# Performance work log

Measured on AMD Instinct MI355X. Metric: run time of the kernel, lower is better.

Reference implementation:

```python
import jax, jax.numpy as jnp
import numpy as np

D_MODEL = 768
D_STATE = 16
K_CONV = 4
BATCH = 2
SEQ = 2048


def setup_inputs() -> dict:
    key = jax.random.key(0)
    ks = jax.random.split(key, 16)
    dm, ds, K = D_MODEL, D_STATE, K_CONV
    s = 0.02
    inp = {
        "x": jax.random.normal(ks[0], (BATCH, SEQ, dm), dtype=jnp.float32),
        # linear weights stored (in, out); y = x @ W + b (equivalent to torch Linear)
        "Wi": jax.random.normal(ks[1], (dm, 2 * dm), dtype=jnp.float32) * s,
        "bi": jnp.zeros((2 * dm,), jnp.float32),
        "Wconv": jax.random.normal(ks[2], (dm, K), dtype=jnp.float32) * s,
        "bconv": jnp.zeros((dm,), jnp.float32),
        "Wdt": jax.random.normal(ks[3], (dm, dm), dtype=jnp.float32) * s,
        "bdt": jnp.zeros((dm,), jnp.float32),
        "WB": jax.random.normal(ks[4], (dm, dm * ds), dtype=jnp.float32) * s,
        "bB": jnp.zeros((dm * ds,), jnp.float32),
        "WC": jax.random.normal(ks[5], (dm, dm * ds), dtype=jnp.float32) * s,
        "bC": jnp.zeros((dm * ds,), jnp.float32),
        "A_log": jnp.zeros((dm, ds), jnp.float32),  # matches nn.Parameter(torch.zeros)
        "D": jnp.ones((dm,), jnp.float32),          # matches nn.Parameter(torch.ones)
        "Wo": jax.random.normal(ks[6], (dm, dm), dtype=jnp.float32) * s,
        "bo": jnp.zeros((dm,), jnp.float32),
    }
    return inp


def _forward(x, Wi, bi, Wconv, bconv, Wdt, bdt, WB, bB, WC, bC, A_log, D, Wo, bo):
    B, L, dm = x.shape
    ds = A_log.shape[1]
    K = Wconv.shape[1]

    uv = x @ Wi + bi                        # (B, L, 2*dm)
    u, v = uv[..., :dm], uv[..., dm:]

    # causal depthwise conv1d: torch pads K-1 both sides, keeps first L outputs
    u_pad = jnp.pad(u, ((0, 0), (K - 1, 0), (0, 0)))
    u_conv = bconv + sum(u_pad[:, k:k + L, :] * Wconv[:, k] for k in range(K))

    dt = jax.nn.softplus(u_conv @ Wdt + bdt)            # (B, L, dm)
    Bt = (u_conv @ WB + bB).reshape(B, L, dm, ds)       # (B, L, dm, ds)
    Ct = (u_conv @ WC + bC).reshape(B, L, dm, ds)
    A = -jnp.exp(A_log)                                  # (dm, ds)

    def step(s, inputs):
        dt_t, u_t, B_tt, C_tt = inputs                   # (B,dm), (B,dm), (B,dm,ds), (B,dm,ds)
        dt_e = dt_t[..., None]
        s = s * jnp.exp(dt_e * A) + dt_e * B_tt * u_t[..., None]
        y = jnp.sum(C_tt * s, axis=-1) + D * u_t         # (B, dm)
        return s, y

    s0 = jnp.zeros((B, dm, ds), x.dtype)
    xs = (dt.transpose(1, 0, 2), u_conv.transpose(1, 0, 2),
          Bt.transpose(1, 0, 2, 3), Ct.transpose(1, 0, 2, 3))
    _, ys = jax.lax.scan(step, s0, xs)                   # ys: (L, B, dm)
    y = ys.transpose(1, 0, 2)

    y = y * jax.nn.sigmoid(v)
    return y @ Wo + bo


def reference(x, Wi, bi, Wconv, bconv, Wdt, bdt, WB, bB, WC, bC, A_log, D, Wo, bo):
    return _forward(x, Wi, bi, Wconv, bconv, Wdt, bdt, WB, bB, WC, bC, A_log, D, Wo, bo)
```

## Files before the change

### kernel.cpp

```cpp
#include <hip/hip_runtime.h>

#define DM 768
#define DS 16
#define SEQ 2048
#define BATCH 2
#define MROWS (BATCH*SEQ)
#define N_UV (2*DM)
#define N_BC (DM*DS)
#define NGRP (BATCH*DM/4)
#define SUBMAX 64

typedef _Float16 half8 __attribute__((ext_vector_type(8)));
typedef float floatx4 __attribute__((ext_vector_type(4)));
typedef int i32x4 __attribute__((ext_vector_type(4)));
typedef unsigned short us8 __attribute__((ext_vector_type(8)));
typedef signed char c8 __attribute__((ext_vector_type(8)));
typedef __fp16 fp16x2 __attribute__((ext_vector_type(2)));

static __device__ __forceinline__ unsigned short f2h(float f) {
  _Float16 h = (_Float16)f;
  return __builtin_bit_cast(unsigned short, h);
}
static __device__ __forceinline__ float h2f(unsigned short u) {
  return (float)__builtin_bit_cast(_Float16, u);
}
static __device__ __forceinline__ unsigned int pk2h(float a, float b) {
  fp16x2 r = __builtin_amdgcn_cvt_pkrtz(a, b);
  return __builtin_bit_cast(unsigned int, r);
}
static __device__ __forceinline__ float softplus_f(float x) {
  return (x > 20.f) ? x : log1pf(__expf(x));
}
static __device__ __forceinline__ void async_cp16(const void* g, void* l) {
  __builtin_amdgcn_global_load_lds(
      (const __attribute__((address_space(1))) void*)g,
      (__attribute__((address_space(3))) void*)l, 16, 0, 0);
}
static __device__ __forceinline__ float row_reduce16(float v) {
  int x;
  x = __builtin_amdgcn_update_dpp(0, __builtin_bit_cast(int, v), 0x128, 0xf, 0xf, true);
  v += __builtin_bit_cast(float, x);
  x = __builtin_amdgcn_update_dpp(0, __builtin_bit_cast(int, v), 0x124, 0xf, 0xf, true);
  v += __builtin_bit_cast(float, x);
  x = __builtin_amdgcn_update_dpp(0, __builtin_bit_cast(int, v), 0x122, 0xf, 0xf, true);
  v += __builtin_bit_cast(float, x);
  x = __builtin_amdgcn_update_dpp(0, __builtin_bit_cast(int, v), 0x121, 0xf, 0xf, true);
  v += __builtin_bit_cast(float, x);
  return v;
}

__global__ void convert_f2h(const float* __restrict__ in,
                            unsigned short* __restrict__ out, int n) {
  int i = (blockIdx.x * blockDim.x + threadIdx.x) * 4;
  if (i >= n) return;
  float4 f = *(const float4*)(in + i);
  ushort4 h;
  h.x = f2h(f.x); h.y = f2h(f.y); h.z = f2h(f.z); h.w = f2h(f.w);
  *(ushort4*)(out + i) = h;
}

__global__ void transpose_w5(const float* __restrict__ W0, const float* __restrict__ W1,
                             const float* __restrict__ W2, const float* __restrict__ W3,
                             const float* __restrict__ W4,
                             unsigned short* __restrict__ T0, unsigned short* __restrict__ T1,
                             unsigned short* __restrict__ T2, unsigned short* __restrict__ T3,
                             unsigned short* __restrict__ T4,
                             int N0, int N1, int N2, int N3, int N4) {
  const float* W; unsigned short* WT; int N;
  switch (blockIdx.z) {
    case 0: W = W0; WT = T0; N = N0; break;
    case 1: W = W1; WT = T1; N = N1; break;
    case 2: W = W2; WT = T2; N = N2; break;
    case 3: W = W3; WT = T3; N = N3; break;
    default: W = W4; WT = T4; N = N4; break;
  }
  int n0 = blockIdx.x * 32;
  if (n0 >= N) return;
  int k0 = blockIdx.y * 32;
  __shared__ float tile[32][33];
  int tx = threadIdx.x, ty = threadIdx.y;
#pragma unroll
  for (int i = 0; i < 32; i += 8)
    tile[ty + i][tx] = W[(size_t)(k0 + ty + i) * N + (n0 + tx)];
  __syncthreads();
  int kp = tx & 15, half = tx >> 4;
#pragma unroll
  for (int i = 0; i < 2; i++) {
    int nl = ty + half * 8 + i * 16;
    unsigned int pk = (unsigned int)f2h(tile[2 * kp][nl]) |
                      ((unsigned int)f2h(tile[2 * kp + 1][nl]) << 16);
    *(unsigned int*)&WT[(size_t)(n0 + nl) * DM + k0 + 2 * kp] = pk;
  }
}

__global__ __launch_bounds__(256)
void quant_rows(const unsigned short* __restrict__ in0,
                const unsigned short* __restrict__ in1,
                signed char* __restrict__ out0, signed char* __restrict__ out1,
                float* __restrict__ sc0, float* __restrict__ sc1, int R) {
  const unsigned short* in = blockIdx.y ? in1 : in0;
  signed char* out = blockIdx.y ? out1 : out0;
  float* scp = blockIdx.y ? sc1 : sc0;
  int row = blockIdx.x * 4 + (threadIdx.x >> 6);
  if (row >= R) return;
  int lane = threadIdx.x & 63;
  const us8* ch = (const us8*)(in + (size_t)row * DM);
  us8 a = ch[lane];
  us8 b = ch[64 + (lane & 31)];
  float fa[8], fb[8];
  float m = 0.f;
#pragma unroll
  for (int j = 0; j < 8; j++) { fa[j] = h2f(a[j]); m = fmaxf(m, fabsf(fa[j])); }
#pragma unroll
  for (int j = 0; j < 8; j++) fb[j] = h2f(b[j]);
  if (lane < 32) {
#pragma unroll
    for (int j = 0; j < 8; j++) m = fmaxf(m, fabsf(fb[j]));
  }
#pragma unroll
  for (int off = 32; off; off >>= 1) m = fmaxf(m, __shfl_xor(m, off));
  float inv = (m > 0.f) ? 127.f / m : 0.f;
  if (lane == 0) scp[row] = m * (1.f / 127.f);
  c8 qa, qb;
#pragma unroll
  for (int j = 0; j < 8; j++)
    qa[j] = (signed char)__float2int_rn(fminf(fmaxf(fa[j] * inv, -127.f), 127.f));
#pragma unroll
  for (int j = 0; j < 8; j++)
    qb[j] = (signed char)__float2int_rn(fminf(fmaxf(fb[j] * inv, -127.f), 127.f));
  c8* o = (c8*)(out + (size_t)row * DM);
  o[lane] = qa;
  if (lane < 32) o[64 + lane] = qb;
}

template<int ACT, int OUTH>
__global__ __launch_bounds__(256)
void gemm_f16(const unsigned short* __restrict__ A,
              const unsigned short* __restrict__ BT0,
              const unsigned short* __restrict__ BT1,
              const float* __restrict__ bias0,
              const float* __restrict__ bias1,
              void* __restrict__ Cout0,
              void* __restrict__ Cout1,
              int M, int N, int K, int TCa, int bstride, int row0) {
  const unsigned short* BT = blockIdx.z ? BT1 : BT0;
  const float* bias = blockIdx.z ? bias1 : bias0;
  void* Cout = blockIdx.z ? Cout1 : Cout0;
  __shared__ __align__(16) unsigned short As[128 * 32];
  __shared__ __align__(16) unsigned short Bs[128 * 32];
  const int m0 = blockIdx.y * 128, n0 = blockIdx.x * 128;
  const int tid = threadIdx.x;
  const int lane = tid & 63, wave = tid >> 6;
  const int wm = (wave >> 1) * 64, wn = (wave & 1) * 64;
  const int l16 = lane & 15, quad = lane >> 4;
  const int sr = tid >> 2;
  const int sc = (((tid & 3) ^ ((tid >> 3) & 3))) * 8;
  const int pch = (quad ^ ((l16 >> 1) & 3)) * 8;

  floatx4 acc[4][4] = {};

  const int mA0 = m0 + sr, mA1 = m0 + sr + 64;
  const int gA0 = (mA0 / TCa) * bstride + row0 + (mA0 % TCa);
  const int gA1 = (mA1 / TCa) * bstride + row0 + (mA1 % TCa);
  const unsigned short* Arow0 = A + (size_t)gA0 * K + sc;
  const unsigned short* Arow1 = A + (size_t)gA1 * K + sc;
  const unsigned short* Brow0 = BT + (size_t)(n0 + sr) * K + sc;
  const unsigned short* Brow1 = BT + (size_t)(n0 + sr + 64) * K + sc;
  unsigned short* ldsA0 = As + (wave * 16) * 32;
  unsigned short* ldsA1 = As + (64 + wave * 16) * 32;
  unsigned short* ldsB0 = Bs + (wave * 16) * 32;
  unsigned short* ldsB1 = Bs + (64 + wave * 16) * 32;

  for (int k0 = 0; k0 < K; k0 += 32) {
    async_cp16(Arow0 + k0, ldsA0);
    async_cp16(Arow1 + k0, ldsA1);
    async_cp16(Brow0 + k0, ldsB0);
    async_cp16(Brow1 + k0, ldsB1);
    __syncthreads();
    half8 af[4], bf[4];
#pragma unroll
    for (int i = 0; i < 4; i++) {
      af[i] = __builtin_bit_cast(half8, *(const uint4*)&As[(wm + i * 16 + l16) * 32 + pch]);
      bf[i] = __builtin_bit_cast(half8, *(const uint4*)&Bs[(wn + i * 16 + l16) * 32 + pch]);
    }
#pragma unroll
    for (int mi = 0; mi < 4; mi++)
#pragma unroll
      for (int ni = 0; ni < 4; ni++)
        acc[mi][ni] = __builtin_amdgcn_mfma_f32_16x16x32_f16(af[mi], bf[ni], acc[mi][ni], 0, 0, 0);
    __syncthreads();
  }

#pragma unroll
  for (int ni = 0; ni < 4; ni++) {
    int col = n0 + wn + ni * 16 + l16;
    float bv = bias[col];
#pragma unroll
    for (int mi = 0; mi < 4; mi++) {
#pragma unroll
      for (int r = 0; r < 4; r++) {
        int row = m0 + wm + mi * 16 + quad * 4 + r;
        float v = acc[mi][ni][r] + bv;
        if (ACT == 1) v = softplus_f(v);
        if (OUTH) ((unsigned short*)Cout)[(size_t)row * N + col] = f2h(v);
        else      ((float*)Cout)[(size_t)row * N + col] = v;
      }
    }
  }
}

__global__ __launch_bounds__(256)
void gemm_i8(const signed char* __restrict__ A,
             const signed char* __restrict__ BT0,
             const signed char* __restrict__ BT1,
             const float* __restrict__ bias0,
             const float* __restrict__ bias1,
             const float* __restrict__ sA,
             const float* __restrict__ sB0,
             const float* __restrict__ sB1,
             unsigned short* __restrict__ C0,
             unsigned short* __restrict__ C1,
             int M, int N, int K, int TCa, int bstride, int row0) {
  const signed char* BT = blockIdx.z ? BT1 : BT0;
  const float* bias = blockIdx.z ? bias1 : bias0;
  const float* sB = blockIdx.z ? sB1 : sB0;
  unsigned short* Cout = blockIdx.z ? C1 : C0;
  __shared__ __align__(16) signed char As[3][128 * 64];
  __shared__ __align__(16) signed char Bs[3][128 * 64];
  const int m0 = blockIdx.y * 128, n0 = blockIdx.x * 128;
  const int tid = threadIdx.x;
  const int lane = tid & 63, wave = tid >> 6;
  const int wm = (wave >> 1) * 64, wn = (wave & 1) * 64;
  const int l16 = lane & 15, quad = lane >> 4;
  const int sr = tid >> 2;
  const int sc = ((tid & 3) ^ ((tid >> 3) & 3)) * 16;
  const int pch = (quad ^ ((l16 >> 1) & 3)) * 16;

  i32x4 acc[4][4] = {};

  const int mA0 = m0 + sr, mA1 = m0 + sr + 64;
  const int gA0 = (mA0 / TCa) * bstride + row0 + (mA0 % TCa);
  const int gA1 = (mA1 / TCa) * bstride + row0 + (mA1 % TCa);
  const signed char* Arow0 = A + (size_t)gA0 * K + sc;
  const signed char* Arow1 = A + (size_t)gA1 * K + sc;
  const signed char* Brow0 = BT + (size_t)(n0 + sr) * K + sc;
  const signed char* Brow1 = BT + (size_t)(n0 + sr + 64) * K + sc;
  const int woff = (wave * 16) * 64;

  const int nt = K >> 6;
  auto stage = [&](int t, int b) {
    int k0 = t << 6;
    async_cp16(Arow0 + k0, &As[b][woff]);
    async_cp16(Arow1 + k0, &As[b][64 * 64 + woff]);
    async_cp16(Brow0 + k0, &Bs[b][woff]);
    async_cp16(Brow1 + k0, &Bs[b][64 * 64 + woff]);
  };
  stage(0, 0);
  if (nt > 1) stage(1, 1);
  int cur = 0;
  for (int t = 0; t < nt; ++t) {
    if (t + 2 < nt) {
      int b2 = cur + 2; if (b2 >= 3) b2 -= 3;
      stage(t + 2, b2);
      asm volatile("s_waitcnt vmcnt(8)" ::: "memory");
    } else if (t + 1 < nt) {
      asm volatile("s_waitcnt vmcnt(4)" ::: "memory");
    } else {
      asm volatile("s_waitcnt vmcnt(0)" ::: "memory");
    }
    __builtin_amdgcn_s_barrier();
    i32x4 af[4], bf[4];
#pragma unroll
    for (int i = 0; i < 4; i++) {
      af[i] = *(const i32x4*)&As[cur][(wm + i * 16 + l16) * 64 + pch];
      bf[i] = *(const i32x4*)&Bs[cur][(wn + i * 16 + l16) * 64 + pch];
    }
    asm volatile("s_waitcnt lgkmcnt(0)" ::: "memory");
    __builtin_amdgcn_s_barrier();
    __builtin_amdgcn_s_setprio(1);
#pragma unroll
    for (int mi = 0; mi < 4; mi++)
#pragma unroll
      for (int ni = 0; ni < 4; ni++)
        acc[mi][ni] = __builtin_amdgcn_mfma_i32_16x16x64_i8(bf[ni], af[mi], acc[mi][ni], 0, 0, 0);
    __builtin_amdgcn_s_setprio(0);
    cur = (cur == 2) ? 0 : cur + 1;
  }

  const int rowAbase = (m0 / TCa) * (bstride - TCa) + row0;

#pragma unroll
  for (int mi = 0; mi < 4; mi++) {
    int row = m0 + wm + mi * 16 + l16;
    float sa = sA[rowAbase + row];
    size_t outb = (size_t)row * N;
#pragma unroll
    for (int ni = 0; ni < 4; ni++) {
      int nb = n0 + wn + ni * 16 + quad * 4;
      float4 sb4 = *(const float4*)&sB[nb];
      float4 bv4 = *(const float4*)&bias[nb];
      float v0 = (float)acc[mi][ni][0] * (sa * sb4.x) + bv4.x;
      float v1 = (float)acc[mi][ni][1] * (sa * sb4.y) + bv4.y;
      float v2 = (float)acc[mi][ni][2] * (sa * sb4.z) + bv4.z;
      float v3 = (float)acc[mi][ni][3] * (sa * sb4.w) + bv4.w;
      uint2 pk;
      pk.x = pk2h(v0, v1);
      pk.y = pk2h(v2, v3);
      *(uint2*)&Cout[outb + nb] = pk;
    }
  }
}

__global__ void dwconv(const unsigned short* __restrict__ uv,
                       const float* __restrict__ Wconv,
                       const float* __restrict__ bconv,
                       unsigned short* __restrict__ uc) {
  int idx = blockIdx.x * 256 + threadIdx.x;
  int c = (idx % (DM / 2)) * 2;
  int row = idx / (DM / 2);
  int t = row & (SEQ - 1);
  float a0 = bconv[c], a1 = bconv[c + 1];
  const float* w0 = Wconv + c * 4;
  const float* w1 = Wconv + (c + 1) * 4;
#pragma unroll
  for (int k = 0; k < 4; k++) {
    int tt = t - 3 + k;
    if (tt >= 0) {
      ushort2 u2 = *(const ushort2*)&uv[(size_t)(row - 3 + k) * N_UV + c];
      a0 += h2f(u2.x) * w0[k];
      a1 += h2f(u2.y) * w1[k];
    }
  }
  ushort2 o; o.x = f2h(a0); o.y = f2h(a1);
  *(ushort2*)&uc[(size_t)row * DM + c] = o;
}

__global__ __launch_bounds__(64)
void scan_pass1(const unsigned short* __restrict__ dt,
                const unsigned short* __restrict__ uc,
                const unsigned short* __restrict__ Btc,
                const float* __restrict__ A_log,
                float* __restrict__ Ssub,
                float* __restrict__ Aexp,
                int ci, int TC, int SUBn) {
  const int TSUB = TC / SUBn;
  int wid = blockIdx.x, sub = blockIdx.y;
  int b = wid / (DM / 4);
  int c0 = (wid % (DM / 4)) * 4;
  int lane = threadIdx.x;
  int c = c0 + (lane >> 4);
  float Acj = -__expf(A_log[c0 * DS + lane]);
  int col = c0 * DS + lane;
  size_t gbase = (size_t)b * SEQ + (size_t)ci * TC + (size_t)sub * TSUB;
  size_t lbase = (size_t)b * TC + (size_t)sub * TSUB;

  float s = 0.f, dsum = 0.f;
  float n_dt[8], n_u[8], n_B[8];
#pragma unroll
  for (int i = 0; i < 8; i++) {
    n_dt[i] = h2f(dt[(gbase + i) * DM + c]);
    n_u[i]  = h2f(uc[(gbase + i) * DM + c]);
    n_B[i]  = h2f(Btc[(lbase + i) * N_BC + col]);
  }
  for (int t0 = 0; t0 < TSUB; t0 += 8) {
    float c_dt[8], c_u[8], c_B[8];
#pragma unroll
    for (int i = 0; i < 8; i++) { c_dt[i] = n_dt[i]; c_u[i] = n_u[i]; c_B[i] = n_B[i]; }
    if (t0 + 8 < TSUB) {
#pragma unroll
      for (int i = 0; i < 8; i++) {
        size_t gr = gbase + t0 + 8 + i, lr = lbase + t0 + 8 + i;
        n_dt[i] = h2f(dt[gr * DM + c]);
        n_u[i]  = h2f(uc[gr * DM + c]);
        n_B[i]  = h2f(Btc[lr * N_BC + col]);
      }
    }
#pragma unroll
    for (int i = 0; i < 8; i++) {
      float dtc = c_dt[i];
      dsum += dtc;
      float a = __expf(dtc * Acj);
      s = fmaf(s, a, dtc * c_B[i] * c_u[i]);
    }
  }
  int idx = (sub * BATCH + b) * N_BC + col;
  Ssub[idx] = s;
  Aexp[idx] = __expf(Acj * dsum);
}

template<int SUBN>
__global__ __launch_bounds__(64)
void scan_combine(const float* Ssub, const float* Aexp,
                  float* Sinit, float* s_state, int ci) {
  int wid = blockIdx.x;
  int b = wid / (DM / 4);
  int c0 = (wid % (DM / 4)) * 4;
  int col = c0 * DS + threadIdx.x;
  int sidx = b * N_BC + col;
  float sa[SUBN], ae[SUBN];
#pragma unroll
  for (int k = 0; k < SUBN; k++) {
    int idx = (k * BATCH + b) * N_BC + col;
    sa[k] = Ssub[idx];
    ae[k] = Aexp[idx];
  }
  float s = (ci == 0) ? 0.f : s_state[sidx];
#pragma unroll
  for (int k = 0; k < SUBN; k++) {
    int idx = (k * BATCH + b) * N_BC + col;
    Sinit[idx] = s;
    s = fmaf(s, ae[k], sa[k]);
  }
  s_state[sidx] = s;
}

__global__ __launch_bounds__(64)
void scan_pass2(const unsigned short* __restrict__ dt,
                const unsigned short* __restrict__ uc,
                const unsigned short* __restrict__ Btc,
                const unsigned short* __restrict__ Ctc,
                const unsigned short* __restrict__ uv,
                const float* __restrict__ A_log,
                const float* __restrict__ Dv,
                const float* __restrict__ Sinit,
                unsigned short* __restrict__ yg,
                int ci, int TC, int SUBn) {
  const int TSUB = TC / SUBn;
  int wid = blockIdx.x, sub = blockIdx.y;
  int b = wid / (DM / 4);
  int c0 = (wid % (DM / 4)) * 4;
  int lane = threadIdx.x;
  int j = lane & 15;
  int c = c0 + (lane >> 4);
  float Acj = -__expf(A_log[c0 * DS + lane]);
  float Dc = Dv[c];
  int col = c0 * DS + lane;
  float s = Sinit[(sub * BATCH + b) * N_BC + col];
  size_t gbase = (size_t)b * SEQ + (size_t)ci * TC + (size_t)sub * TSUB;
  size_t lbase = (size_t)b * TC + (size_t)sub * TSUB;

  float n_dt[8], n_u[8], n_B[8], n_C[8], n_v[8];
#pragma unroll
  for (int i = 0; i < 8; i++) {
    size_t gr = gbase + i, lr = lbase + i;
    n_dt[i] = h2f(dt[gr * DM + c]);
    n_u[i]  = h2f(uc[gr * DM + c]);
    n_B[i]  = h2f(Btc[lr * N_BC + col]);
    n_C[i]  = h2f(Ctc[lr * N_BC + col]);
    n_v[i]  = h2f(uv[gr * N_UV + DM + c]);
  }
  for (int t0 = 0; t0 < TSUB; t0 += 8) {
    float c_dt[8], c_u[8], c_B[8], c_C[8], c_v[8];
#pragma unroll
    for (int i = 0; i < 8; i++) {
      c_dt[i] = n_dt[i]; c_u[i] = n_u[i]; c_B[i] = n_B[i];
      c_C[i] = n_C[i]; c_v[i] = n_v[i];
    }
    if (t0 + 8 < TSUB) {
#pragma unroll
      for (int i = 0; i < 8; i++) {
        size_t gr = gbase + t0 + 8 + i, lr = lbase + t0 + 8 + i;
        n_dt[i] = h2f(dt[gr * DM + c]);
        n_u[i]  = h2f(uc[gr * DM + c]);
        n_B[i]  = h2f(Btc[lr * N_BC + col]);
        n_C[i]  = h2f(Ctc[lr * N_BC + col]);
        n_v[i]  = h2f(uv[gr * N_UV + DM + c]);
      }
    }
#pragma unroll
    for (int i = 0; i < 8; i++) {
      float dtc = c_dt[i];
      float a = __expf(dtc * Acj);
      s = fmaf(s, a, dtc * c_B[i] * c_u[i]);
      float yt = row_reduce16(c_C[i] * s);
      if (j == 0) {
        float y = yt + Dc * c_u[i];
        float g = 1.f / (1.f + __expf(-c_v[i]));
        yg[(gbase + t0 + i) * DM + c] = f2h(y * g);
      }
    }
  }
}

extern "C" void kernel_launch(void* const* d_in, const int* in_sizes, int n_in,
                              void* d_out, int out_size, void* d_ws, size_t ws_size,
                              hipStream_t stream) {
  const float* x     = (const float*)d_in[0];
  const float* Wi    = (const float*)d_in[1];
  const float* bi    = (const float*)d_in[2];
  const float* Wconv = (const float*)d_in[3];
  const float* bconv = (const float*)d_in[4];
  const float* Wdt   = (const float*)d_in[5];
  const float* bdt   = (const float*)d_in[6];
  const float* WB    = (const float*)d_in[7];
  const float* bB    = (const float*)d_in[8];
  const float* WC    = (const float*)d_in[9];
  const float* bC    = (const float*)d_in[10];
  const float* A_log = (const float*)d_in[11];
  const float* Dv    = (const float*)d_in[12];
  const float* Wo    = (const float*)d_in[13];
  const float* bo    = (const float*)d_in[14];
  float* out = (float*)d_out;
  (void)in_sizes; (void)n_in; (void)out_size;

  auto pad = [](size_t b) { return (b + 255) & ~(size_t)255; };

  const size_t sz_xb   = pad((size_t)MROWS * DM * 2);
  const size_t sz_WiT  = pad((size_t)N_UV * DM * 2);
  const size_t sz_WdtT = pad((size_t)DM * DM * 2);
  const size_t sz_WBT  = pad((size_t)N_BC * DM * 2);
  const size_t sz_WCT  = pad((size_t)N_BC * DM * 2);
  const size_t sz_WoT  = pad((size_t)DM * DM * 2);
  const size_t sz_uvb  = pad((size_t)MROWS * N_UV * 2);
  const size_t sz_ucb  = pad((size_t)MROWS * DM * 2);
  const size_t sz_dtb  = pad((size_t)MROWS * DM * 2);
  const size_t sz_st   = pad((size_t)BATCH * N_BC * 4);
  const size_t sz_sub  = pad((size_t)SUBMAX * BATCH * N_BC * 4);
  const size_t sz_uc8  = pad((size_t)MROWS * DM);
  const size_t sz_w8   = pad((size_t)N_BC * DM);
  const size_t sz_sA   = pad((size_t)MROWS * 4);
  const size_t sz_sB   = pad((size_t)N_BC * 4);
  const size_t fixed = sz_xb + sz_WiT + sz_WdtT + sz_WBT + sz_WCT + sz_WoT +
                       sz_uvb + sz_ucb + sz_dtb + sz_st + 2 * sz_sub +
                       sz_uc8 + 2 * sz_w8 + sz_sA + 2 * sz_sB;

  int NC = 16;
  for (int nc : {1, 2, 4, 8, 16}) {
    size_t need = fixed + 2 * pad((size_t)BATCH * (SEQ / nc) * N_BC * 2);
    if (need <= ws_size) { NC = nc; break; }
  }
  const int TC = SEQ / NC;
  const int MC = BATCH * TC;
  const int SUBn = (TC / 8 < SUBMAX) ? (TC / 8) : SUBMAX;

  char* ws = (char*)d_ws;
  size_t off = 0;
  auto alloc = [&](size_t bytes) { char* p = ws + off; off += bytes; return p; };
  unsigned short* xb   = (unsigned short*)alloc(sz_xb);
  unsigned short* WiT  = (unsigned short*)alloc(sz_WiT);
  unsigned short* WdtT = (unsigned short*)alloc(sz_WdtT);
  unsigned short* WBT  = (unsigned short*)alloc(sz_WBT);
  unsigned short* WCT  = (unsigned short*)alloc(sz_WCT);
  unsigned short* WoT  = (unsigned short*)alloc(sz_WoT);
  unsigned short* uvb  = (unsigned short*)alloc(sz_uvb);
  unsigned short* ucb  = (unsigned short*)alloc(sz_ucb);
  unsigned short* dtb  = (unsigned short*)alloc(sz_dtb);
  float*          sst  = (float*)alloc(sz_st);
  float*          Ssub = (float*)alloc(sz_sub);
  float*          Aexp = (float*)alloc(sz_sub);
  signed char*    uc8  = (signed char*)alloc(sz_uc8);
  signed char*    WBT8 = (signed char*)alloc(sz_w8);
  signed char*    WCT8 = (signed char*)alloc(sz_w8);
  float*          sAu  = (float*)alloc(sz_sA);
  float*          sB0  = (float*)alloc(sz_sB);
  float*          sB1  = (float*)alloc(sz_sB);
  unsigned short* Btc  = (unsigned short*)alloc(pad((size_t)MC * N_BC * 2));
  unsigned short* Ctc  = (unsigned short*)alloc(pad((size_t)MC * N_BC * 2));
  unsigned short* ygb  = xb;
  float*          Sini = Ssub;

  convert_f2h<<<dim3(MROWS * DM / 1024), dim3(256), 0, stream>>>(x, xb, MROWS * DM);
  transpose_w5<<<dim3(N_BC / 32, DM / 32, 5), dim3(32, 8), 0, stream>>>(
      Wi, Wdt, WB, WC, Wo, WiT, WdtT, WBT, WCT, WoT, N_UV, DM, N_BC, N_BC, DM);
  quant_rows<<<dim3(N_BC / 4, 2), 256, 0, stream>>>(WBT, WCT, WBT8, WCT8,
                                                    sB0, sB1, N_BC);

  gemm_f16<0, 1><<<dim3(N_UV / 128, MROWS / 128, 1), 256, 0, stream>>>(
      xb, WiT, WiT, bi, bi, uvb, uvb, MROWS, N_UV, DM, MROWS, 0, 0);
  dwconv<<<dim3(MROWS * DM / 512), 256, 0, stream>>>(uvb, Wconv, bconv, ucb);
  quant_rows<<<dim3(MROWS / 4, 1), 256, 0, stream>>>(ucb, ucb, uc8, uc8,
                                                     sAu, sAu, MROWS);
  gemm_f16<1, 1><<<dim3(DM / 128, MROWS / 128, 1), 256, 0, stream>>>(
      ucb, WdtT, WdtT, bdt, bdt, dtb, dtb, MROWS, DM, DM, MROWS, 0, 0);

  for (int ci = 0; ci < NC; ci++) {
    gemm_i8<<<dim3(N_BC / 128, MC / 128, 2), 256, 0, stream>>>(
        uc8, WBT8, WCT8, bB, bC, sAu, sB0, sB1, Btc, Ctc,
        MC, N_BC, DM, TC, SEQ, ci * TC);
    scan_pass1<<<dim3(NGRP, SUBn), 64, 0, stream>>>(dtb, ucb, Btc, A_log,
                                                    Ssub, Aexp, ci, TC, SUBn);
    switch (SUBn) {
      case 64: scan_combine<64><<<dim3(NGRP), 64, 0, stream>>>(Ssub, Aexp, Sini, sst, ci); break;
      case 32: scan_combine<32><<<dim3(NGRP), 64, 0, stream>>>(Ssub, Aexp, Sini, sst, ci); break;
      default: scan_combine<16><<<dim3(NGRP), 64, 0, stream>>>(Ssub, Aexp, Sini, sst, ci); break;
    }
    scan_pass2<<<dim3(NGRP, SUBn), 64, 0, stream>>>(dtb, ucb, Btc, Ctc, uvb,
                                                    A_log, Dv, Sini, ygb, ci, TC, SUBn);
  }

  gemm_f16<0, 0><<<dim3(DM / 128, MROWS / 128, 1), 256, 0, stream>>>(
      ygb, WoT, WoT, bo, bo, out, out, MROWS, DM, DM, MROWS, 0, 0);
}
```

Baseline: 584.9 us.

## Double-buffer f16 GEMM loads, shrink i8 GEMM to two stages, pack scan waves

The f16 GEMM moves from a single LDS buffer to double buffering, so the global-to-LDS copy for the next K tile is issued before the current tile's MFMAs. It also raises wave priority during the MFMA block. The int8 GEMM goes from a three-stage ring to two buffers with one barrier per iteration, cutting LDS use but shortening the prefetch distance. The scan kernels now pack four 64-lane groups into each 256-thread block, reducing the block count and per-block launch overhead.

```diff
diff --git a/kernel.cpp b/kernel.cpp
--- a/kernel.cpp
+++ b/kernel.cpp
@@ -146,8 +146,8 @@
   const unsigned short* BT = blockIdx.z ? BT1 : BT0;
   const float* bias = blockIdx.z ? bias1 : bias0;
   void* Cout = blockIdx.z ? Cout1 : Cout0;
-  __shared__ __align__(16) unsigned short As[128 * 32];
-  __shared__ __align__(16) unsigned short Bs[128 * 32];
+  __shared__ __align__(16) unsigned short As[2][128 * 32];
+  __shared__ __align__(16) unsigned short Bs[2][128 * 32];
   const int m0 = blockIdx.y * 128, n0 = blockIdx.x * 128;
   const int tid = threadIdx.x;
   const int lane = tid & 63, wave = tid >> 6;
@@ -166,29 +166,40 @@
   const unsigned short* Arow1 = A + (size_t)gA1 * K + sc;
   const unsigned short* Brow0 = BT + (size_t)(n0 + sr) * K + sc;
   const unsigned short* Brow1 = BT + (size_t)(n0 + sr + 64) * K + sc;
-  unsigned short* ldsA0 = As + (wave * 16) * 32;
-  unsigned short* ldsA1 = As + (64 + wave * 16) * 32;
-  unsigned short* ldsB0 = Bs + (wave * 16) * 32;
-  unsigned short* ldsB1 = Bs + (64 + wave * 16) * 32;
-
-  for (int k0 = 0; k0 < K; k0 += 32) {
-    async_cp16(Arow0 + k0, ldsA0);
-    async_cp16(Arow1 + k0, ldsA1);
-    async_cp16(Brow0 + k0, ldsB0);
-    async_cp16(Brow1 + k0, ldsB1);
-    __syncthreads();
+  const int woff = (wave * 16) * 32;
+
+  const int nt = K >> 5;
+  auto stage = [&](int t, int b) {
+    int k0 = t << 5;
+    async_cp16(Arow0 + k0, &As[b][woff]);
+    async_cp16(Arow1 + k0, &As[b][64 * 32 + woff]);
+    async_cp16(Brow0 + k0, &Bs[b][woff]);
+    async_cp16(Brow1 + k0, &Bs[b][64 * 32 + woff]);
+  };
+  stage(0, 0);
+  asm volatile("s_waitcnt vmcnt(0)" ::: "memory");
+  __builtin_amdgcn_s_barrier();
+  int cur = 0;
+  for (int t = 0; t < nt; ++t) {
+    if (t + 1 < nt) stage(t + 1, cur ^ 1);
     half8 af[4], bf[4];
 #pragma unroll
     for (int i = 0; i < 4; i++) {
-      af[i] = __builtin_bit_cast(half8, *(const uint4*)&As[(wm + i * 16 + l16) * 32 + pch]);
-      bf[i] = __builtin_bit_cast(half8, *(const uint4*)&Bs[(wn + i * 16 + l16) * 32 + pch]);
-    }
+      af[i] = __builtin_bit_cast(half8, *(const uint4*)&As[cur][(wm + i * 16 + l16) * 32 + pch]);
+      bf[i] = __builtin_bit_cast(half8, *(const uint4*)&Bs[cur][(wn + i * 16 + l16) * 32 + pch]);
+    }
+    asm volatile("s_waitcnt lgkmcnt(0)" ::: "memory");
+    __builtin_amdgcn_sched_barrier(0);
+    __builtin_amdgcn_s_setprio(1);
 #pragma unroll
     for (int mi = 0; mi < 4; mi++)
 #pragma unroll
       for (int ni = 0; ni < 4; ni++)
         acc[mi][ni] = __builtin_amdgcn_mfma_f32_16x16x32_f16(af[mi], bf[ni], acc[mi][ni], 0, 0, 0);
-    __syncthreads();
+    __builtin_amdgcn_s_setprio(0);
+    asm volatile("s_waitcnt vmcnt(0)" ::: "memory");
+    __builtin_amdgcn_s_barrier();
+    cur ^= 1;
   }
 
 #pragma unroll
@@ -225,8 +236,8 @@
   const float* bias = blockIdx.z ? bias1 : bias0;
   const float* sB = blockIdx.z ? sB1 : sB0;
   unsigned short* Cout = blockIdx.z ? C1 : C0;
-  __shared__ __align__(16) signed char As[3][128 * 64];
-  __shared__ __align__(16) signed char Bs[3][128 * 64];
+  __shared__ __align__(16) signed char As[2][128 * 64];
+  __shared__ __align__(16) signed char Bs[2][128 * 64];
   const int m0 = blockIdx.y * 128, n0 = blockIdx.x * 128;
   const int tid = threadIdx.x;
   const int lane = tid & 63, wave = tid >> 6;
@@ -256,19 +267,11 @@
     async_cp16(Brow1 + k0, &Bs[b][64 * 64 + woff]);
   };
   stage(0, 0);
-  if (nt > 1) stage(1, 1);
+  asm volatile("s_waitcnt vmcnt(0)" ::: "memory");
+  __builtin_amdgcn_s_barrier();
   int cur = 0;
   for (int t = 0; t < nt; ++t) {
-    if (t + 2 < nt) {
-      int b2 = cur + 2; if (b2 >= 3) b2 -= 3;
-      stage(t + 2, b2);
-      asm volatile("s_waitcnt vmcnt(8)" ::: "memory");
-    } else if (t + 1 < nt) {
-      asm volatile("s_waitcnt vmcnt(4)" ::: "memory");
-    } else {
-      asm volatile("s_waitcnt vmcnt(0)" ::: "memory");
-    }
-    __builtin_amdgcn_s_barrier();
+    if (t + 1 < nt) stage(t + 1, cur ^ 1);
     i32x4 af[4], bf[4];
 #pragma unroll
     for (int i = 0; i < 4; i++) {
@@ -276,7 +279,7 @@
       bf[i] = *(const i32x4*)&Bs[cur][(wn + i * 16 + l16) * 64 + pch];
     }
     asm volatile("s_waitcnt lgkmcnt(0)" ::: "memory");
-    __builtin_amdgcn_s_barrier();
+    __builtin_amdgcn_sched_barrier(0);
     __builtin_amdgcn_s_setprio(1);
 #pragma unroll
     for (int mi = 0; mi < 4; mi++)
@@ -284,7 +287,9 @@
       for (int ni = 0; ni < 4; ni++)
         acc[mi][ni] = __builtin_amdgcn_mfma_i32_16x16x64_i8(bf[ni], af[mi], acc[mi][ni], 0, 0, 0);
     __builtin_amdgcn_s_setprio(0);
-    cur = (cur == 2) ? 0 : cur + 1;
+    asm volatile("s_waitcnt vmcnt(0)" ::: "memory");
+    __builtin_amdgcn_s_barrier();
+    cur ^= 1;
   }
 
   const int rowAbase = (m0 / TCa) * (bstride - TCa) + row0;
@@ -335,7 +340,7 @@
   *(ushort2*)&uc[(size_t)row * DM + c] = o;
 }
 
-__global__ __launch_bounds__(64)
+__global__ __launch_bounds__(256)
 void scan_pass1(const unsigned short* __restrict__ dt,
                 const unsigned short* __restrict__ uc,
                 const unsigned short* __restrict__ Btc,
@@ -344,10 +349,11 @@
                 float* __restrict__ Aexp,
                 int ci, int TC, int SUBn) {
   const int TSUB = TC / SUBn;
-  int wid = blockIdx.x, sub = blockIdx.y;
+  int wid = blockIdx.x * 4 + (threadIdx.x >> 6);
+  int sub = blockIdx.y;
   int b = wid / (DM / 4);
   int c0 = (wid % (DM / 4)) * 4;
-  int lane = threadIdx.x;
+  int lane = threadIdx.x & 63;
   int c = c0 + (lane >> 4);
   float Acj = -__expf(A_log[c0 * DS + lane]);
   int col = c0 * DS + lane;
@@ -389,13 +395,14 @@
 }
 
 template<int SUBN>
-__global__ __launch_bounds__(64)
+__global__ __launch_bounds__(256)
 void scan_combine(const float* Ssub, const float* Aexp,
                   float* Sinit, float* s_state, int ci) {
-  int wid = blockIdx.x;
+  int wid = blockIdx.x * 4 + (threadIdx.x >> 6);
+  int lane = threadIdx.x & 63;
   int b = wid / (DM / 4);
   int c0 = (wid % (DM / 4)) * 4;
-  int col = c0 * DS + threadIdx.x;
+  int col = c0 * DS + lane;
   int sidx = b * N_BC + col;
   float sa[SUBN], ae[SUBN];
 #pragma unroll
@@ -414,7 +421,7 @@
   s_state[sidx] = s;
 }
 
-__global__ __launch_bounds__(64)
+__global__ __launch_bounds__(256)
 void scan_pass2(const unsigned short* __restrict__ dt,
                 const unsigned short* __restrict__ uc,
                 const unsigned short* __restrict__ Btc,
@@ -426,10 +433,11 @@
                 unsigned short* __restrict__ yg,
                 int ci, int TC, int SUBn) {
   const int TSUB = TC / SUBn;
-  int wid = blockIdx.x, sub = blockIdx.y;
+  int wid = blockIdx.x * 4 + (threadIdx.x >> 6);
+  int sub = blockIdx.y;
   int b = wid / (DM / 4);
   int c0 = (wid % (DM / 4)) * 4;
-  int lane = threadIdx.x;
+  int lane = threadIdx.x & 63;
   int j = lane & 15;
   int c = c0 + (lane >> 4);
   float Acj = -__expf(A_log[c0 * DS + lane]);
@@ -577,15 +585,15 @@
     gemm_i8<<<dim3(N_BC / 128, MC / 128, 2), 256, 0, stream>>>(
         uc8, WBT8, WCT8, bB, bC, sAu, sB0, sB1, Btc, Ctc,
         MC, N_BC, DM, TC, SEQ, ci * TC);
-    scan_pass1<<<dim3(NGRP, SUBn), 64, 0, stream>>>(dtb, ucb, Btc, A_log,
-                                                    Ssub, Aexp, ci, TC, SUBn);
+    scan_pass1<<<dim3(NGRP / 4, SUBn), 256, 0, stream>>>(dtb, ucb, Btc, A_log,
+                                                         Ssub, Aexp, ci, TC, SUBn);
     switch (SUBn) {
-      case 64: scan_combine<64><<<dim3(NGRP), 64, 0, stream>>>(Ssub, Aexp, Sini, sst, ci); break;
-      case 32: scan_combine<32><<<dim3(NGRP), 64, 0, stream>>>(Ssub, Aexp, Sini, sst, ci); break;
-      default: scan_combine<16><<<dim3(NGRP), 64, 0, stream>>>(Ssub, Aexp, Sini, sst, ci); break;
-    }
-    scan_pass2<<<dim3(NGRP, SUBn), 64, 0, stream>>>(dtb, ucb, Btc, Ctc, uvb,
-                                                    A_log, Dv, Sini, ygb, ci, TC, SUBn);
+      case 64: scan_combine<64><<<dim3(NGRP / 4), 256, 0, stream>>>(Ssub, Aexp, Sini, sst, ci); break;
+      case 32: scan_combine<32><<<dim3(NGRP / 4), 256, 0, stream>>>(Ssub, Aexp, Sini, sst, ci); break;
+      default: scan_combine<16><<<dim3(NGRP / 4), 256, 0, stream>>>(Ssub, Aexp, Sini, sst, ci); break;
+    }
+    scan_pass2<<<dim3(NGRP / 4, SUBn), 256, 0, stream>>>(dtb, ucb, Btc, Ctc, uvb,
+                                                         A_log, Dv, Sini, ygb, ci, TC, SUBn);
   }
 
   gemm_f16<0, 0><<<dim3(DM / 128, MROWS / 128, 1), 256, 0, stream>>>(
```

Result: no change. 576.0 us (-1.5%).
